# Kernel optimization log

Hardware: AMD Instinct MI355X
Metric: run time of the kernel (lower is better)

The kernel has to match this reference:

```python
import jax, jax.numpy as jnp
import numpy as np

N, DIN, DOUT, R, H = 3072, 128, 128, 3, 4


def setup_inputs() -> dict:
    key = jax.random.key(0)
    k0, k1, k2, k3 = jax.random.split(key, 4)
    features = jax.random.normal(k0, (N, DIN), jnp.float32)
    adjacency = jax.random.randint(k1, (R, N, N), 0, 2, jnp.int32)
    W = jax.random.normal(k2, (R, DOUT, DIN), jnp.float32) * (1.0 / np.sqrt(DIN))  # Linear weights (out,in)
    hd = DOUT // H
    a = jax.random.normal(k3, (R, 2 * hd), jnp.float32) * (1.0 / np.sqrt(2 * hd))  # attention vectors
    bias = jnp.zeros((DOUT,), jnp.float32)
    return {"features": features, "adjacency": adjacency, "W": W, "a": a,
            "bias": bias, "num_heads": H}


def reference(features, adjacency, W, a, bias, num_heads):
    # features: [N, Din], adjacency: [R, N, N] int, W: [R, Dout, Din],
    # a: [R, 2*head_dim], bias: [Dout]
    Rr, Dout = W.shape[0], W.shape[1]
    Nn = features.shape[0]
    hd = Dout // num_heads
    # per-relation linear transform -> [R, N, H, hd]
    t = jnp.einsum('nd,rod->rno', features, W).reshape(Rr, Nn, num_heads, hd)
    # additive attention: score(i,j,h) = a_src . t[i,h] + a_dst . t[j,h]
    s_src = jnp.einsum('rnhd,rd->rnh', t, a[:, :hd])
    s_dst = jnp.einsum('rnhd,rd->rnh', t, a[:, hd:])
    mask = (adjacency != 0)[..., None]  # [R, N, N, 1]
    # original fills NON-edges with 0 (not -inf), then softmaxes over j incl. zeros
    scores = jnp.where(mask, s_src[:, :, None, :] + s_dst[:, None, :, :], 0.0)  # [R,N,N,H]
    w = jax.nn.softmax(scores, axis=2)
    # aggregation only sums over true edges
    w = jnp.where(mask, w, 0.0)
    out = jnp.einsum('rijh,rjhd->rihd', w, t).reshape(Rr, Nn, Dout)
    return out.mean(axis=0) + bias
```

## Files before the change

kernel.cpp:

```cpp
#include <hip/hip_runtime.h>

typedef float  f32x4  __attribute__((ext_vector_type(4)));
typedef float  f32x2  __attribute__((ext_vector_type(2)));
typedef short  bf16x8 __attribute__((ext_vector_type(8)));
typedef int    i32x4  __attribute__((ext_vector_type(4)));

#define NNODE 3072
#define DIN   128
#define DOUT  128
#define NREL  3
#define NH    4
#define HD    32
#define KCH   48
#define CHB   9216

static __device__ __forceinline__ unsigned short f2bf(float v) {
  unsigned u = __builtin_bit_cast(unsigned, v);
  u += 0x7FFFu + ((u >> 16) & 1u);
  return (unsigned short)(u >> 16);
}

__global__ __launch_bounds__(256, 1) void k0_init(
    const float* __restrict__ bias, float* __restrict__ out)
{
  const int tid = blockIdx.x * 256 + threadIdx.x;
  f32x4 b = *(const f32x4*)(bias + (tid & 31) * 4);
  *((f32x4*)out + tid) = b;
}

__global__ __launch_bounds__(256, 1) void k1_prep(
    const float* __restrict__ feat, const float* __restrict__ W,
    const float* __restrict__ av, unsigned short* __restrict__ Mt,
    float* __restrict__ Es)
{
  const int jt = blockIdx.x;
  const int r  = blockIdx.y;
  const int t  = threadIdx.x;
  const int jb = jt * 64;

  __shared__ float Wl[128 * 130];
  __shared__ float Fl[64 * 129];
  __shared__ float Tl[64 * 129];
  __shared__ float El[64 * 5];

  const float* Wr = W + r * DOUT * DIN;
  for (int idx = t * 4; idx < DOUT * DIN; idx += 1024) {
    float4 v = *(const float4*)(Wr + idx);
    int o = idx >> 7, k = idx & 127;
    float* d = Wl + o * 130 + k;
    d[0] = v.x; d[1] = v.y; d[2] = v.z; d[3] = v.w;
  }
  for (int idx = t * 4; idx < 64 * DIN; idx += 1024) {
    float4 v = *(const float4*)(feat + (size_t)jb * DIN + idx);
    int n = idx >> 7, k = idx & 127;
    float* d = Fl + n * 129 + k;
    d[0] = v.x; d[1] = v.y; d[2] = v.z; d[3] = v.w;
  }
  __syncthreads();

  {
    const int ng = t & 15, og = t >> 4;
    float acc[4][8] = {};
    for (int k = 0; k < DIN; k += 4) {
      float wv[4][8];
      #pragma unroll
      for (int oo = 0; oo < 8; ++oo) {
        const float* wr2 = Wl + (og * 8 + oo) * 130 + k;
        f32x2 a01 = *(const f32x2*)wr2;
        f32x2 a23 = *(const f32x2*)(wr2 + 2);
        wv[0][oo] = a01[0]; wv[1][oo] = a01[1];
        wv[2][oo] = a23[0]; wv[3][oo] = a23[1];
      }
      #pragma unroll
      for (int nn = 0; nn < 4; ++nn) {
        const float* fr = Fl + (ng * 4 + nn) * 129 + k;
        float f0 = fr[0], f1 = fr[1], f2 = fr[2], f3 = fr[3];
        #pragma unroll
        for (int oo = 0; oo < 8; ++oo) {
          float s = acc[nn][oo];
          s = fmaf(f0, wv[0][oo], s);
          s = fmaf(f1, wv[1][oo], s);
          s = fmaf(f2, wv[2][oo], s);
          s = fmaf(f3, wv[3][oo], s);
          acc[nn][oo] = s;
        }
      }
    }
    #pragma unroll
    for (int nn = 0; nn < 4; ++nn)
      #pragma unroll
      for (int oo = 0; oo < 8; ++oo)
        Tl[(ng * 4 + nn) * 129 + og * 8 + oo] = acc[nn][oo];
  }
  __syncthreads();

  {
    const int n = t & 63, h = t >> 6;
    const float* tr = Tl + n * 129 + h * HD;
    const float* as = av + r * 2 * HD;
    float ss = 0.f, sd = 0.f;
    #pragma unroll
    for (int d = 0; d < HD; ++d) {
      float tvv = tr[d];
      ss = fmaf(tvv, as[d],      ss);
      sd = fmaf(tvv, as[HD + d], sd);
    }
    Es[((size_t)r * NNODE + jb + n) * NH + h] = expf(ss);
    El[n * 5 + h] = expf(sd);
  }
  __syncthreads();

  {
    const int n = t & 63, cb = t >> 6;
    unsigned short* base = Mt + ((size_t)r * KCH + jt) * CHB;
    const int s = n >> 5, k8 = (n >> 3) & 3, elem = n & 7;
    const int lanebase = k8 * 16;
    #pragma unroll
    for (int ci = 0; ci < 36; ++ci) {
      int c = cb * 36 + ci;
      float v;
      if (c < DOUT)            v = Tl[n * 129 + c] * El[n * 5 + (c >> 5)];
      else if (c < DOUT + NH)  v = El[n * 5 + (c - DOUT)];
      else if (c == DOUT + NH) v = 1.0f;
      else                     v = 0.0f;
      int nt = c >> 4;
      base[(nt * 2 + s) * 512 + (lanebase + (c & 15)) * 8 + elem] = f2bf(v);
    }
  }
}

__global__ __launch_bounds__(256, 3) void k2_agg(
    const int* __restrict__ adj, const unsigned short* __restrict__ Mt,
    const float* __restrict__ Es, float* __restrict__ out)
{
  const int it = blockIdx.x;
  const int r  = blockIdx.y;
  const int t  = threadIdx.x;
  const int wv = t >> 6;
  const int l  = t & 63;
  const int l16 = l & 15, l4 = l >> 4;
  const int ib = it * 16;

  __shared__ __align__(16) int Ash[4][2][1024];
  __shared__ float red[16 * 145];
  __shared__ float coefL[64];

  const size_t adjBase = (size_t)r * NNODE * NNODE + (size_t)ib * NNODE;
  const int* asrc[4];
  #pragma unroll
  for (int q = 0; q < 4; ++q) {
    int row = q * 4 + l4;
    int chk = l16 ^ (row & 7);
    asrc[q] = adj + adjBase + (size_t)row * NNODE + wv * 64 + chk * 4;
  }
  const unsigned short* bp = Mt + (size_t)r * KCH * CHB + (size_t)wv * CHB + (size_t)l * 8;

  f32x4 acc[9] = {};
  bf16x8 B[9][2];
  int zero = 0;

  #define STAGE(bufi) do {                                                        \
    _Pragma("unroll")                                                             \
    for (int q = 0; q < 4; ++q)                                                   \
      __builtin_amdgcn_global_load_lds(                                           \
        (const __attribute__((address_space(1))) void*)asrc[q],                   \
        (__attribute__((address_space(3))) void*)&Ash[wv][bufi][q * 256], 16, 0, 0); \
  } while (0)

  STAGE(0);

  #pragma unroll 1
  for (int k = 0; k < 12; ++k) {
    #pragma unroll
    for (int ti = 0; ti < 9; ++ti) {
      B[ti][0] = *(const bf16x8*)(bp + (ti * 2 + 0) * 512);
      B[ti][1] = *(const bf16x8*)(bp + (ti * 2 + 1) * 512);
    }
    bp += 4 * CHB;
    __builtin_amdgcn_sched_barrier(0);

    const int adv = (k < 11) ? 256 : 0;
    #pragma unroll
    for (int q = 0; q < 4; ++q) asrc[q] += adv;
    STAGE((k + 1) & 1);

    asm volatile("s_waitcnt vmcnt(4)" : "+v"(zero));
    __builtin_amdgcn_sched_barrier(0);

    const int* Ab = (const int*)((const char*)&Ash[wv][k & 1][0] + zero);
    #pragma unroll
    for (int s = 0; s < 2; ++s) {
      const int ko = s * 32 + l4 * 8;
      const int xm = (l & 7) << 2;
      i32x4 a0 = *(const i32x4*)&Ab[l16 * 64 + ((ko + 0) ^ xm)];
      i32x4 a1 = *(const i32x4*)&Ab[l16 * 64 + ((ko + 4) ^ xm)];
      bf16x8 af = __builtin_bit_cast(bf16x8, (i32x4){
        (a0[0] | (a0[1] << 16)) * 0x3F80, (a0[2] | (a0[3] << 16)) * 0x3F80,
        (a1[0] | (a1[1] << 16)) * 0x3F80, (a1[2] | (a1[3] << 16)) * 0x3F80 });
      #pragma unroll
      for (int ti = 0; ti < 9; ++ti)
        acc[ti] = __builtin_amdgcn_mfma_f32_16x16x32_bf16(af, B[ti][s], acc[ti], 0, 0, 0);
    }
  }

  if (wv == 0) {
    #pragma unroll
    for (int ti = 0; ti < 9; ++ti)
      #pragma unroll
      for (int rg = 0; rg < 4; ++rg)
        red[(l4 * 4 + rg) * 145 + ti * 16 + l16] = acc[ti][rg];
  }
  __syncthreads();
  #pragma unroll 1
  for (int w = 1; w < 4; ++w) {
    if (wv == w) {
      #pragma unroll
      for (int ti = 0; ti < 9; ++ti)
        #pragma unroll
        for (int rg = 0; rg < 4; ++rg)
          red[(l4 * 4 + rg) * 145 + ti * 16 + l16] += acc[ti][rg];
    }
    __syncthreads();
  }

  if (t < 64) {
    int row = t >> 2, h = t & 3;
    float es = Es[((size_t)r * NNODE + ib + row) * NH + h];
    float V  = red[row * 145 + DOUT + h];
    float dg = red[row * 145 + DOUT + NH];
    coefL[t] = es / fmaf(es, V, (float)NNODE - dg) * (1.0f / NREL);
  }
  __syncthreads();

  #pragma unroll
  for (int idx = t; idx < 16 * DOUT; idx += 256) {
    int row = idx >> 7, c = idx & 127;
    atomicAdd(&out[(size_t)(ib + row) * DOUT + c],
              coefL[row * 4 + (c >> 5)] * red[row * 145 + c]);
  }
  #undef STAGE
}

extern "C" void kernel_launch(void* const* d_in, const int* in_sizes, int n_in,
                              void* d_out, int out_size, void* d_ws, size_t ws_size,
                              hipStream_t stream) {
  const float* feat = (const float*)d_in[0];
  const int*   adj  = (const int*)d_in[1];
  const float* W    = (const float*)d_in[2];
  const float* av   = (const float*)d_in[3];
  const float* bias = (const float*)d_in[4];

  char* ws = (char*)d_ws;
  unsigned short* Mt = (unsigned short*)ws;
  float* Es = (float*)(ws + 2654208);

  hipLaunchKernelGGL(k0_init, dim3(384), dim3(256), 0, stream, bias, (float*)d_out);
  hipLaunchKernelGGL(k1_prep, dim3(48, 3), dim3(256), 0, stream, feat, W, av, Mt, Es);
  hipLaunchKernelGGL(k2_agg,  dim3(192, 3), dim3(256), 0, stream, adj, Mt, Es, (float*)d_out);
}
```

Baseline: 64.86 us.

## Split aggregation by output tiles across waves with shared LDS-staged B chunks

The aggregation kernel changes how work is split across waves. Before, each wave took its own K-slice over all 9 output tiles and the partial sums were reduced through LDS. Now all waves walk the full K range together, each wave owns two output column tiles (wave 0 also owns the ninth), and the M chunk is staged cooperatively into double-buffered LDS with global_load_lds. The A tile is triple-buffered with a block-wide barrier each step. This removes the serialized cross-wave reduction and the per-wave redundant B register loads, but adds 48 block barriers, a larger LDS footprint, a drop to 2 blocks per CU, and an imbalance because wave 0 does an extra MFMA.

Result: slower. 106.7 us (+64.5%).

```diff
diff --git a/kernel.cpp b/kernel.cpp
--- a/kernel.cpp
+++ b/kernel.cpp
@@ -129,7 +129,7 @@
   }
 }
 
-__global__ __launch_bounds__(256, 3) void k2_agg(
+__global__ __launch_bounds__(256, 2) void k2_agg(
     const int* __restrict__ adj, const unsigned short* __restrict__ Mt,
     const float* __restrict__ Es, float* __restrict__ out)
 {
@@ -141,87 +141,87 @@
   const int l16 = l & 15, l4 = l >> 4;
   const int ib = it * 16;
 
-  __shared__ __align__(16) int Ash[4][2][1024];
+  __shared__ __align__(16) int            Abuf[3][1024];
+  __shared__ __align__(16) unsigned short Bbuf[2][CHB];
   __shared__ float red[16 * 145];
   __shared__ float coefL[64];
 
   const size_t adjBase = (size_t)r * NNODE * NNODE + (size_t)ib * NNODE;
-  const int* asrc[4];
-  #pragma unroll
-  for (int q = 0; q < 4; ++q) {
-    int row = q * 4 + l4;
-    int chk = l16 ^ (row & 7);
-    asrc[q] = adj + adjBase + (size_t)row * NNODE + wv * 64 + chk * 4;
-  }
-  const unsigned short* bp = Mt + (size_t)r * KCH * CHB + (size_t)wv * CHB + (size_t)l * 8;
-
-  f32x4 acc[9] = {};
-  bf16x8 B[9][2];
-  int zero = 0;
-
-  #define STAGE(bufi) do {                                                        \
+  const int arow = t >> 4;
+  const int* asrc = adj + adjBase + (size_t)arow * NNODE + ((t & 15) ^ (arow & 7)) * 4;
+
+  const unsigned short* msrc = Mt + (size_t)r * KCH * CHB;
+
+  #define STAGE_A(kc, buf)                                                        \
+    __builtin_amdgcn_global_load_lds(                                             \
+        (const __attribute__((address_space(1))) void*)(asrc + (kc) * 64),        \
+        (__attribute__((address_space(3))) void*)&Abuf[buf][t * 4], 16, 0, 0)
+
+  #define STAGE_B(kc, buf) do {                                                   \
+    const unsigned short* bs_ = msrc + (size_t)(kc) * CHB;                        \
     _Pragma("unroll")                                                             \
-    for (int q = 0; q < 4; ++q)                                                   \
+    for (int j_ = 0; j_ < 4; ++j_)                                                \
       __builtin_amdgcn_global_load_lds(                                           \
-        (const __attribute__((address_space(1))) void*)asrc[q],                   \
-        (__attribute__((address_space(3))) void*)&Ash[wv][bufi][q * 256], 16, 0, 0); \
+        (const __attribute__((address_space(1))) void*)(bs_ + (j_ * 256 + t) * 8),\
+        (__attribute__((address_space(3))) void*)&Bbuf[buf][(j_ * 256 + t) * 8],  \
+        16, 0, 0);                                                                \
+    if (t < 128)                                                                  \
+      __builtin_amdgcn_global_load_lds(                                           \
+        (const __attribute__((address_space(1))) void*)(bs_ + (1024 + t) * 8),    \
+        (__attribute__((address_space(3))) void*)&Bbuf[buf][(1024 + t) * 8],      \
+        16, 0, 0);                                                                \
   } while (0)
 
-  STAGE(0);
+  const int tb = wv * 2;
+  f32x4 acc0 = {}, acc1 = {}, acc2 = {};
+  const int xm = (l & 7) << 2;
+
+  STAGE_A(0, 0);
+  STAGE_B(0, 0);
+  STAGE_A(1, 1);
 
   #pragma unroll 1
-  for (int k = 0; k < 12; ++k) {
-    #pragma unroll
-    for (int ti = 0; ti < 9; ++ti) {
-      B[ti][0] = *(const bf16x8*)(bp + (ti * 2 + 0) * 512);
-      B[ti][1] = *(const bf16x8*)(bp + (ti * 2 + 1) * 512);
-    }
-    bp += 4 * CHB;
+  for (int k = 0; k < KCH; ++k) {
+    asm volatile("s_waitcnt vmcnt(1)");
     __builtin_amdgcn_sched_barrier(0);
-
-    const int adv = (k < 11) ? 256 : 0;
-    #pragma unroll
-    for (int q = 0; q < 4; ++q) asrc[q] += adv;
-    STAGE((k + 1) & 1);
-
-    asm volatile("s_waitcnt vmcnt(4)" : "+v"(zero));
+    __builtin_amdgcn_s_barrier();
     __builtin_amdgcn_sched_barrier(0);
 
-    const int* Ab = (const int*)((const char*)&Ash[wv][k & 1][0] + zero);
+    {
+      const int nb = (k + 1 < KCH) ? k + 1 : KCH - 1;
+      const int na = (k + 2 < KCH) ? k + 2 : KCH - 1;
+      STAGE_B(nb, (k + 1) & 1);
+      STAGE_A(na, (k + 2) % 3);
+    }
+
+    const int ab = k % 3, bb = k & 1;
     #pragma unroll
     for (int s = 0; s < 2; ++s) {
       const int ko = s * 32 + l4 * 8;
-      const int xm = (l & 7) << 2;
-      i32x4 a0 = *(const i32x4*)&Ab[l16 * 64 + ((ko + 0) ^ xm)];
-      i32x4 a1 = *(const i32x4*)&Ab[l16 * 64 + ((ko + 4) ^ xm)];
+      i32x4 a0 = *(const i32x4*)&Abuf[ab][l16 * 64 + ((ko + 0) ^ xm)];
+      i32x4 a1 = *(const i32x4*)&Abuf[ab][l16 * 64 + ((ko + 4) ^ xm)];
       bf16x8 af = __builtin_bit_cast(bf16x8, (i32x4){
         (a0[0] | (a0[1] << 16)) * 0x3F80, (a0[2] | (a0[3] << 16)) * 0x3F80,
         (a1[0] | (a1[1] << 16)) * 0x3F80, (a1[2] | (a1[3] << 16)) * 0x3F80 });
-      #pragma unroll
-      for (int ti = 0; ti < 9; ++ti)
-        acc[ti] = __builtin_amdgcn_mfma_f32_16x16x32_bf16(af, B[ti][s], acc[ti], 0, 0, 0);
-    }
-  }
-
-  if (wv == 0) {
-    #pragma unroll
-    for (int ti = 0; ti < 9; ++ti)
-      #pragma unroll
-      for (int rg = 0; rg < 4; ++rg)
-        red[(l4 * 4 + rg) * 145 + ti * 16 + l16] = acc[ti][rg];
-  }
-  __syncthreads();
-  #pragma unroll 1
-  for (int w = 1; w < 4; ++w) {
-    if (wv == w) {
-      #pragma unroll
-      for (int ti = 0; ti < 9; ++ti)
-        #pragma unroll
-        for (int rg = 0; rg < 4; ++rg)
-          red[(l4 * 4 + rg) * 145 + ti * 16 + l16] += acc[ti][rg];
-    }
-    __syncthreads();
-  }
+      bf16x8 b0 = *(const bf16x8*)&Bbuf[bb][((tb + 0) * 2 + s) * 512 + l * 8];
+      acc0 = __builtin_amdgcn_mfma_f32_16x16x32_bf16(af, b0, acc0, 0, 0, 0);
+      bf16x8 b1 = *(const bf16x8*)&Bbuf[bb][((tb + 1) * 2 + s) * 512 + l * 8];
+      acc1 = __builtin_amdgcn_mfma_f32_16x16x32_bf16(af, b1, acc1, 0, 0, 0);
+      if (wv == 0) {
+        bf16x8 b2 = *(const bf16x8*)&Bbuf[bb][(8 * 2 + s) * 512 + l * 8];
+        acc2 = __builtin_amdgcn_mfma_f32_16x16x32_bf16(af, b2, acc2, 0, 0, 0);
+      }
+    }
+  }
+
+  #pragma unroll
+  for (int rg = 0; rg < 4; ++rg) {
+    red[(l4 * 4 + rg) * 145 + (tb + 0) * 16 + l16] = acc0[rg];
+    red[(l4 * 4 + rg) * 145 + (tb + 1) * 16 + l16] = acc1[rg];
+    if (wv == 0)
+      red[(l4 * 4 + rg) * 145 + 8 * 16 + l16] = acc2[rg];
+  }
+  __syncthreads();
 
   if (t < 64) {
     int row = t >> 2, h = t & 3;
@@ -238,7 +238,8 @@
     atomicAdd(&out[(size_t)(ib + row) * DOUT + c],
               coefL[row * 4 + (c >> 5)] * red[row * 145 + c]);
   }
-  #undef STAGE
+  #undef STAGE_A
+  #undef STAGE_B
 }
 
 extern "C" void kernel_launch(void* const* d_in, const int* in_sizes, int n_in,
```

## Pack adjacency into bitmasks in a separate pass before aggregation

Applied to the files above, without the earlier changes.

Adds a pre-pass that converts the int32 adjacency into 1-bit masks with wave ballots, so the aggregation kernel reads a compact bitmask instead of full int32 rows. The aggregation kernel is restructured to work on 32-row tiles, split output columns across waves, and double-buffer the B operand in registers with inline-asm loads, expanding bits to bf16 with byte permutes. The full adjacency still has to be read once, but only by a streaming kernel. In exchange the change adds an extra launch and a round trip through workspace, and falls back to the old kernel when the workspace is too small.

Measured after the change: 78.77 us. +21.4%, slower.

```diff
diff --git a/kernel.cpp b/kernel.cpp
--- a/kernel.cpp
+++ b/kernel.cpp
@@ -129,7 +129,145 @@
   }
 }
 
-__global__ __launch_bounds__(256, 3) void k2_agg(
+__global__ __launch_bounds__(256) void k2a_pack(
+    const int* __restrict__ adj, unsigned int* __restrict__ pk)
+{
+  const int wgid = blockIdx.x * 4 + (threadIdx.x >> 6);
+  const int l = threadIdx.x & 63;
+  #pragma unroll 1
+  for (int i = 0; i < 54; ++i) {
+    const int u = i * 8192 + wgid;
+    const int rrow = u / 48, c64 = u - rrow * 48;
+    int a = adj[(size_t)rrow * NNODE + c64 * 64 + l];
+    unsigned long long m = __ballot(a != 0);
+    if (l == 0)
+      *(unsigned long long*)(pk + (size_t)rrow * 96 + c64 * 2) = m;
+  }
+}
+
+#define GLO(dst, p, off) \
+  asm volatile("global_load_dwordx4 %0, %1, off offset:" off : "=v"(dst) : "v"(p))
+
+#define EXPAND(d, dst) do {                                                \
+    unsigned b_  = ((d) >> sh) & 0xFFu;                                    \
+    unsigned lo_ = ((b_ & 0x0Fu) * 0x204081u) & 0x01010101u;               \
+    unsigned hi_ = ((b_ >> 4)   * 0x204081u) & 0x01010101u;                \
+    dst = __builtin_bit_cast(bf16x8, (i32x4){                              \
+      (int)(__builtin_amdgcn_perm(0u, lo_, 0x0C010C00u) * 0x3F80u),        \
+      (int)(__builtin_amdgcn_perm(0u, lo_, 0x0C030C02u) * 0x3F80u),        \
+      (int)(__builtin_amdgcn_perm(0u, hi_, 0x0C010C00u) * 0x3F80u),        \
+      (int)(__builtin_amdgcn_perm(0u, hi_, 0x0C030C02u) * 0x3F80u)});      \
+  } while (0)
+
+#define MF(a, b, c) __builtin_amdgcn_mfma_f32_16x16x32_bf16(a, __builtin_bit_cast(bf16x8, b), c, 0, 0, 0)
+
+__global__ __launch_bounds__(256, 2) void k2b_agg(
+    const unsigned int* __restrict__ pk, const unsigned short* __restrict__ Mt,
+    const float* __restrict__ Es, float* __restrict__ out)
+{
+  const int it = blockIdx.x;
+  const int r  = blockIdx.y;
+  const int t  = threadIdx.x;
+  const int wv = t >> 6;
+  const int l  = t & 63;
+  const int l16 = l & 15, l4 = l >> 4;
+  const int ib = it * 32;
+  const bool w3 = (wv == 3);
+  const unsigned sh = (unsigned)l4 * 8u;
+
+  __shared__ unsigned Al[32 * 97];
+  __shared__ float red[32 * 145];
+  __shared__ float coefL[128];
+
+  {
+    const unsigned* pg = pk + ((size_t)r * NNODE + ib) * 96;
+    #pragma unroll
+    for (int x = 0; x < 12; ++x) {
+      int idx = t + x * 256;
+      Al[(idx / 96) * 97 + (idx % 96)] = pg[idx];
+    }
+  }
+  __syncthreads();
+
+  const unsigned short* bpw = Mt + (size_t)r * KCH * CHB + (size_t)(wv * 4) * 512 + (size_t)l * 8;
+
+  i32x4 A0={},A1={},A2={},A3={},A4={},A5={};
+  i32x4 B0={},B1={},B2={},B3={},B4={},B5={};
+  f32x4 acc00={}, acc01={}, acc10={}, acc11={}, acc20={}, acc21={};
+
+  {
+    const unsigned short* p0 = bpw;
+    GLO(A0, p0, "0"); GLO(A1, p0, "1024"); GLO(A2, p0, "2048"); GLO(A3, p0, "3072");
+    if (w3) { const unsigned short* p4 = p0 + 2048; GLO(A4, p4, "0"); GLO(A5, p4, "1024"); }
+  }
+
+  #define STEP(kc, X0,X1,X2,X3,X4,X5, Y0,Y1,Y2,Y3,Y4,Y5) do {              \
+    const int nk_ = ((kc) + 1 < KCH) ? (kc) + 1 : KCH - 1;                  \
+    const unsigned short* np_ = bpw + (size_t)nk_ * CHB;                    \
+    GLO(Y0, np_, "0"); GLO(Y1, np_, "1024");                                \
+    GLO(Y2, np_, "2048"); GLO(Y3, np_, "3072");                             \
+    if (w3) { const unsigned short* n4_ = np_ + 2048;                       \
+              GLO(Y4, n4_, "0"); GLO(Y5, n4_, "1024"); }                    \
+    const int c2_ = 2 * (kc);                                               \
+    unsigned d00_ = Al[l16 * 97 + c2_],        d01_ = Al[l16 * 97 + c2_ + 1]; \
+    unsigned d10_ = Al[(16 + l16) * 97 + c2_], d11_ = Al[(16 + l16) * 97 + c2_ + 1]; \
+    bf16x8 af0_, af1_;                                                      \
+    EXPAND(d00_, af0_); EXPAND(d10_, af1_);                                 \
+    if (w3) { asm volatile("s_waitcnt vmcnt(6)"                             \
+        : "+v"(X0), "+v"(X1), "+v"(X2), "+v"(X3), "+v"(X4), "+v"(X5)); }    \
+    else    { asm volatile("s_waitcnt vmcnt(4)"                             \
+        : "+v"(X0), "+v"(X1), "+v"(X2), "+v"(X3)); }                        \
+    __builtin_amdgcn_sched_barrier(0);                                      \
+    acc00 = MF(af0_, X0, acc00); acc01 = MF(af1_, X0, acc01);               \
+    acc10 = MF(af0_, X2, acc10); acc11 = MF(af1_, X2, acc11);               \
+    if (w3) { acc20 = MF(af0_, X4, acc20); acc21 = MF(af1_, X4, acc21); }   \
+    EXPAND(d01_, af0_); EXPAND(d11_, af1_);                                 \
+    acc00 = MF(af0_, X1, acc00); acc01 = MF(af1_, X1, acc01);               \
+    acc10 = MF(af0_, X3, acc10); acc11 = MF(af1_, X3, acc11);               \
+    if (w3) { acc20 = MF(af0_, X5, acc20); acc21 = MF(af1_, X5, acc21); }   \
+  } while (0)
+
+  #pragma unroll 1
+  for (int k = 0; k < KCH; k += 2) {
+    STEP(k,     A0,A1,A2,A3,A4,A5,  B0,B1,B2,B3,B4,B5);
+    STEP(k + 1, B0,B1,B2,B3,B4,B5,  A0,A1,A2,A3,A4,A5);
+  }
+  asm volatile("s_waitcnt vmcnt(0)"
+      : "+v"(A0), "+v"(A1), "+v"(A2), "+v"(A3), "+v"(A4), "+v"(A5));
+  #undef STEP
+
+  const int tc0 = wv * 2;
+  #pragma unroll
+  for (int j = 0; j < 4; ++j) {
+    red[(l4 * 4 + j) * 145 + (tc0 + 0) * 16 + l16]      = acc00[j];
+    red[(16 + l4 * 4 + j) * 145 + (tc0 + 0) * 16 + l16] = acc01[j];
+    red[(l4 * 4 + j) * 145 + (tc0 + 1) * 16 + l16]      = acc10[j];
+    red[(16 + l4 * 4 + j) * 145 + (tc0 + 1) * 16 + l16] = acc11[j];
+    if (w3) {
+      red[(l4 * 4 + j) * 145 + 8 * 16 + l16]      = acc20[j];
+      red[(16 + l4 * 4 + j) * 145 + 8 * 16 + l16] = acc21[j];
+    }
+  }
+  __syncthreads();
+
+  if (t < 128) {
+    int row = t >> 2, h = t & 3;
+    float es = Es[((size_t)r * NNODE + ib + row) * NH + h];
+    float V  = red[row * 145 + DOUT + h];
+    float dg = red[row * 145 + DOUT + NH];
+    coefL[t] = es / fmaf(es, V, (float)NNODE - dg) * (1.0f / NREL);
+  }
+  __syncthreads();
+
+  #pragma unroll
+  for (int idx = t; idx < 32 * DOUT; idx += 256) {
+    int row = idx >> 7, c = idx & 127;
+    atomicAdd(&out[(size_t)(ib + row) * DOUT + c],
+              coefL[row * 4 + (c >> 5)] * red[row * 145 + c]);
+  }
+}
+
+__global__ __launch_bounds__(256, 3) void k2_fb(
     const int* __restrict__ adj, const unsigned short* __restrict__ Mt,
     const float* __restrict__ Es, float* __restrict__ out)
 {
@@ -202,6 +340,7 @@
         acc[ti] = __builtin_amdgcn_mfma_f32_16x16x32_bf16(af, B[ti][s], acc[ti], 0, 0, 0);
     }
   }
+  #undef STAGE
 
   if (wv == 0) {
     #pragma unroll
@@ -238,7 +377,6 @@
     atomicAdd(&out[(size_t)(ib + row) * DOUT + c],
               coefL[row * 4 + (c >> 5)] * red[row * 145 + c]);
   }
-  #undef STAGE
 }
 
 extern "C" void kernel_launch(void* const* d_in, const int* in_sizes, int n_in,
@@ -253,8 +391,14 @@
   char* ws = (char*)d_ws;
   unsigned short* Mt = (unsigned short*)ws;
   float* Es = (float*)(ws + 2654208);
+  unsigned int* pk = (unsigned int*)(ws + 2801664);
 
   hipLaunchKernelGGL(k0_init, dim3(384), dim3(256), 0, stream, bias, (float*)d_out);
   hipLaunchKernelGGL(k1_prep, dim3(48, 3), dim3(256), 0, stream, feat, W, av, Mt, Es);
-  hipLaunchKernelGGL(k2_agg,  dim3(192, 3), dim3(256), 0, stream, adj, Mt, Es, (float*)d_out);
-}
+  if (ws_size >= 6340608) {
+    hipLaunchKernelGGL(k2a_pack, dim3(2048), dim3(256), 0, stream, adj, pk);
+    hipLaunchKernelGGL(k2b_agg,  dim3(96, 3), dim3(256), 0, stream, pk, Mt, Es, (float*)d_out);
+  } else {
+    hipLaunchKernelGGL(k2_fb, dim3(192, 3), dim3(256), 0, stream, adj, Mt, Es, (float*)d_out);
+  }
+}
```
